# Optimization experiments

Hardware: AMD Instinct MI355X
Metric: run time of the kernel (lower is better)

Reference implementation:

```python
import jax, jax.numpy as jnp
import numpy as np

K = 5
TAU = 2.0
EPS = 1e-8
SLOPE = 0.2  # LeakyReLU negative slope
BASE = jnp.array([-2.0, -1.0, 0.0, 1.0, 2.0], dtype=jnp.float32)


def _leaky(x):
    return jnp.where(x >= 0, x, SLOPE * x)


def _bilinear1d(feat, x):
    """1D bilinear sample, equivalent to F.grid_sample on an [B,C,1,L] image
    with grid_y=0, padding_mode='border', align_corners=True.
    feat: [B,C,L], x: [B,M] normalized coords in [-1,1]. Returns [B,C,M]."""
    L = feat.shape[-1]
    ix = jnp.clip((x + 1.0) * 0.5 * (L - 1), 0.0, float(L - 1))  # border clamp
    x0 = jnp.floor(ix)
    w = (ix - x0)[:, None, :]  # [B,1,M]
    i0 = jnp.clip(x0.astype(jnp.int32), 0, L - 1)
    i1 = jnp.clip(i0 + 1, 0, L - 1)
    f0 = jnp.take_along_axis(feat, i0[:, None, :], axis=2)
    f1 = jnp.take_along_axis(feat, i1[:, None, :], axis=2)
    return f0 * (1.0 - w) + f1 * w


def setup_inputs() -> dict:
    key = jax.random.key(0)
    ks = jax.random.split(key, 10)
    B, C, Lin, N, H = 4, 256, 4096, 8192, 64
    out_dim = 1 + 1 + K + K  # 12
    feat_1d = jax.random.normal(ks[0], (B, C, Lin), dtype=jnp.float32)
    coords_1d = jax.random.uniform(ks[1], (B, N, 1), minval=-1.0, maxval=1.0, dtype=jnp.float32)
    cell_1d = jnp.full((B, N, 1), 2.0 / Lin, dtype=jnp.float32) * (1.0 + 0.1 * jax.random.uniform(ks[2], (B, N, 1)))
    in_dim = C + 2
    # NOTE: original zero-inits the last linear; we use small random weights to
    # exercise the full computation (non-degenerate offsets/gates).
    W1 = jax.random.normal(ks[3], (in_dim, H), dtype=jnp.float32) * (1.0 / np.sqrt(in_dim))
    b1 = jax.random.normal(ks[4], (H,), dtype=jnp.float32) * 0.01
    Wr = jax.random.normal(ks[5], (H, H), dtype=jnp.float32) * (1.0 / np.sqrt(H))
    br = jax.random.normal(ks[6], (H,), dtype=jnp.float32) * 0.01
    W3 = jax.random.normal(ks[7], (H, out_dim), dtype=jnp.float32) * 0.1
    b3 = jax.random.normal(ks[8], (out_dim,), dtype=jnp.float32) * 0.01
    return {"feat_1d": feat_1d, "coords_1d": coords_1d, "cell_1d": cell_1d,
            "W1": W1, "b1": b1, "Wr": Wr, "br": br, "W3": W3, "b3": b3}


def reference(feat_1d, coords_1d, cell_1d, W1, b1, Wr, br, W3, b3):
    B, C, Lin = feat_1d.shape
    N = coords_1d.shape[1]
    x = coords_1d[..., 0]  # [B,N]
    # anchor features at query coords
    f_anchor = _bilinear1d(feat_1d, x).transpose(0, 2, 1)  # [B,N,C]
    rin = jnp.concatenate([f_anchor, coords_1d, cell_1d], axis=-1)  # [B,N,C+2]
    # router MLP: Linear -> LeakyReLU -> ResidualBlock -> Linear
    h = _leaky(rin @ W1 + b1)
    h = _leaky(h + (h @ Wr + br))
    out = h @ W3 + b3  # [B,N,12]
    r_raw = out[..., 0:1]
    sigma_raw = out[..., 1:2]
    res_raw = out[..., 2:2 + K]
    gate_raw = out[..., 2 + K:2 + 2 * K]
    r = jnp.clip(jax.nn.softplus(r_raw) + 0.3, 0.3, 2.0)          # [B,N,1]
    sigma = jnp.clip(jax.nn.softplus(sigma_raw) + 0.5, 0.5, 3.0)  # [B,N,1]
    res = jnp.tanh(res_raw) * 0.5                                  # [B,N,K]
    off = r * BASE + res                                           # [B,N,K] pixel-unit offsets
    scale_x = 2.0 / max(Lin - 1, 1)
    deform_x = x[:, :, None] + off * scale_x                       # [B,N,K] normalized
    f = _bilinear1d(feat_1d, deform_x.reshape(B, N * K))           # [B,C,N*K]
    f = f.reshape(B, C, N, K).transpose(0, 2, 3, 1)                # [B,N,K,C]
    w_geo = jnp.exp(-0.5 * off ** 2 / ((sigma * TAU) ** 2 + EPS))  # [B,N,K]
    w = w_geo * jax.nn.sigmoid(gate_raw)
    w = w / (w.sum(axis=-1, keepdims=True) + EPS)
    out_feat = jnp.einsum('bnkc,bnk->bnc', f, w)                   # [B,N,C]
    return out_feat
```

## Files before the change

### kernel.cpp

```cpp
#include <hip/hip_runtime.h>
#include <math.h>

#define KK 5
#define C_DIM 256
#define LIN 4096
#define B_DIM 4
#define N_PTS 8192
#define PTS 32
#define NBUCK (B_DIM * LIN)
#define WROWS 32
#define SROWS 44

typedef short short8 __attribute__((ext_vector_type(8)));
typedef float f32x4  __attribute__((ext_vector_type(4)));

__device__ __forceinline__ float leaky(float v) { return v >= 0.0f ? v : 0.2f * v; }
__device__ __forceinline__ float softplus_f(float v) { return v > 20.0f ? v : log1pf(expf(v)); }
__device__ __forceinline__ float bflo(unsigned u) { return __uint_as_float(u << 16); }
__device__ __forceinline__ float bfhi(unsigned u) { return __uint_as_float(u & 0xFFFF0000u); }
__device__ __forceinline__ ushort f2bf(float f) {
    unsigned u = __float_as_uint(f);
    u += 0x7FFFu + ((u >> 16) & 1u);
    return (ushort)(u >> 16);
}
__device__ __forceinline__ float bf2f(ushort h) { return __uint_as_float((unsigned)h << 16); }
__device__ __forceinline__ int anchor_key(const float* coords, int pt) {
    float x = coords[pt];
    float ix = fminf(fmaxf((x + 1.0f) * 0.5f * (float)(LIN - 1), 0.0f), (float)(LIN - 1));
    return (pt >> 13) * LIN + (int)ix;
}

__global__ __launch_bounds__(256) void prep_weights(
    const float* __restrict__ W1, const float* __restrict__ Wr,
    ushort* __restrict__ W1t_hi, ushort* __restrict__ W1t_lo,
    ushort* __restrict__ Wrt_hi, ushort* __restrict__ Wrt_lo)
{
    int i = blockIdx.x * 256 + threadIdx.x;
    if (i < 64 * 264) {
        int j = i / 264, k = i % 264;
        float v = (k < 256) ? W1[(size_t)k * 64 + j] : 0.0f;
        ushort hi = f2bf(v);
        W1t_hi[i] = hi;
        W1t_lo[i] = f2bf(v - bf2f(hi));
    } else {
        int i2 = i - 64 * 264;
        if (i2 < 64 * 72) {
            int j = i2 / 72, k = i2 % 72;
            float v = (k < 64) ? Wr[(size_t)k * 64 + j] : 0.0f;
            ushort hi = f2bf(v);
            Wrt_hi[i2] = hi;
            Wrt_lo[i2] = f2bf(v - bf2f(hi));
        }
    }
}

__global__ __launch_bounds__(256) void sort_count(
    const float* __restrict__ coords, unsigned* __restrict__ hist)
{
    int pt = blockIdx.x * 256 + threadIdx.x;
    atomicAdd(&hist[anchor_key(coords, pt)], 1u);
}

__global__ __launch_bounds__(256) void sort_scan(
    const unsigned* __restrict__ hist, unsigned* __restrict__ offs,
    unsigned* __restrict__ pfx)
{
    __shared__ unsigned base[256];
    int t = threadIdx.x;
    unsigned s = 0;
    for (int i = 0; i < NBUCK / 256; i++) s += hist[t * (NBUCK / 256) + i];
    base[t] = s;
    __syncthreads();
    if (t == 0) {
        unsigned run = 0;
        for (int i = 0; i < 256; i++) { unsigned v = base[i]; base[i] = run; run += v; }
    }
    __syncthreads();
    unsigned run = base[t];
    for (int i = 0; i < NBUCK / 256; i++) {
        int idx = t * (NBUCK / 256) + i;
        offs[idx] = run;
        pfx[idx] = run;
        run += hist[idx];
    }
    if (t == 255) pfx[NBUCK] = run;
}

__global__ __launch_bounds__(256) void sort_scatter(
    const float* __restrict__ coords, unsigned* __restrict__ offs,
    int* __restrict__ perm)
{
    int pt = blockIdx.x * 256 + threadIdx.x;
    unsigned pos = atomicAdd(&offs[anchor_key(coords, pt)], 1u);
    perm[pos] = pt;
}

__global__ __launch_bounds__(256) void transpose_kernel(
    const float* __restrict__ feat, ushort* __restrict__ feat_t)
{
    __shared__ float tile[64][33];
    int b  = blockIdx.z;
    int l0 = blockIdx.x * 32;
    int c0 = blockIdx.y * 64;
    const float* src = feat + (size_t)b * C_DIM * LIN;
    unsigned* dst = (unsigned*)(feat_t + (size_t)b * LIN * C_DIM);
    int tx = threadIdx.x, ty = threadIdx.y;
#pragma unroll
    for (int i = 0; i < 8; i++)
        tile[ty + i * 8][tx] = src[(size_t)(c0 + ty + i * 8) * LIN + (l0 + tx)];
    __syncthreads();
#pragma unroll
    for (int i = 0; i < 4; i++) {
        int l = ty + i * 8;
        unsigned lo = f2bf(tile[2 * tx][l]);
        unsigned hi = f2bf(tile[2 * tx + 1][l]);
        dst[((size_t)(l0 + l) * C_DIM + c0) / 2 + tx] = lo | (hi << 16);
    }
}

__global__ __launch_bounds__(256) void mlp_kernel(
    const ushort* __restrict__ feat_t,
    const float* __restrict__ coords,
    const float* __restrict__ cell,
    const float* __restrict__ W1, const float* __restrict__ b1,
    const float* __restrict__ br,
    const float* __restrict__ W3, const float* __restrict__ b3,
    const ushort* __restrict__ W1t_hi, const ushort* __restrict__ W1t_lo,
    const ushort* __restrict__ Wrt_hi, const ushort* __restrict__ Wrt_lo,
    const int* __restrict__ perm,
    float* __restrict__ params)
{
    __shared__ ushort Ah[PTS][264], Al[PTS][264];
    __shared__ ushort H1h[PTS][72], H1l[PTS][72];
    __shared__ float  H2[PTS][68];
    __shared__ float  outs[PTS][12];
    __shared__ float  xs[PTS], cls[PTS];

    const int t = threadIdx.x;
    const int base = blockIdx.x * PTS;
    const int bb = base >> 13;
    const ushort* fb = feat_t + (size_t)bb * LIN * C_DIM;

    {
        int p = t >> 3, l8 = t & 7;
        int pt = perm[base + p];
        float x = coords[pt];
        float ix = fminf(fmaxf((x + 1.0f) * 0.5f * (float)(LIN - 1), 0.0f), (float)(LIN - 1));
        float x0 = floorf(ix);
        int i0 = min((int)x0, LIN - 1);
        int i1 = min(i0 + 1, LIN - 1);
        float fr = ix - x0, om = 1.0f - fr;
        if (l8 == 0) { xs[p] = x; cls[p] = cell[pt]; }
        const ushort* r0 = fb + (size_t)i0 * C_DIM;
        const ushort* r1 = fb + (size_t)i1 * C_DIM;
#pragma unroll
        for (int q = 0; q < 4; q++) {
            int c = l8 * 8 + q * 64;
            uint4 u0 = *(const uint4*)(r0 + c);
            uint4 u1 = *(const uint4*)(r1 + c);
            float v[8];
            v[0] = bflo(u0.x) * om + bflo(u1.x) * fr;
            v[1] = bfhi(u0.x) * om + bfhi(u1.x) * fr;
            v[2] = bflo(u0.y) * om + bflo(u1.y) * fr;
            v[3] = bfhi(u0.y) * om + bfhi(u1.y) * fr;
            v[4] = bflo(u0.z) * om + bflo(u1.z) * fr;
            v[5] = bfhi(u0.z) * om + bfhi(u1.z) * fr;
            v[6] = bflo(u0.w) * om + bflo(u1.w) * fr;
            v[7] = bfhi(u0.w) * om + bfhi(u1.w) * fr;
            ushort hv[8], lv[8];
#pragma unroll
            for (int e = 0; e < 8; e++) {
                hv[e] = f2bf(v[e]);
                lv[e] = f2bf(v[e] - bf2f(hv[e]));
            }
            *(uint4*)&Ah[p][c] = *(uint4*)hv;
            *(uint4*)&Al[p][c] = *(uint4*)lv;
        }
    }
    __syncthreads();

    const int wave = t >> 6, lane = t & 63;
    const int cr = lane & 15;
    const int kb = lane >> 4;
    const int jcol = wave * 16 + cr;

    f32x4 acc0 = {0.f, 0.f, 0.f, 0.f}, acc1 = acc0;
    {
        const ushort* B1h = W1t_hi + (size_t)jcol * 264;
        const ushort* B1l = W1t_lo + (size_t)jcol * 264;
#pragma unroll
        for (int k0 = 0; k0 < 256; k0 += 32) {
            int ko = k0 + kb * 8;
            short8 a0h = *(const short8*)&Ah[cr][ko];
            short8 a0l = *(const short8*)&Al[cr][ko];
            short8 a1h = *(const short8*)&Ah[16 + cr][ko];
            short8 a1l = *(const short8*)&Al[16 + cr][ko];
            short8 bh = *(const short8*)(B1h + ko);
            short8 bl = *(const short8*)(B1l + ko);
            acc0 = __builtin_amdgcn_mfma_f32_16x16x32_bf16(a0h, bh, acc0, 0, 0, 0);
            acc0 = __builtin_amdgcn_mfma_f32_16x16x32_bf16(a0h, bl, acc0, 0, 0, 0);
            acc0 = __builtin_amdgcn_mfma_f32_16x16x32_bf16(a0l, bh, acc0, 0, 0, 0);
            acc1 = __builtin_amdgcn_mfma_f32_16x16x32_bf16(a1h, bh, acc1, 0, 0, 0);
            acc1 = __builtin_amdgcn_mfma_f32_16x16x32_bf16(a1h, bl, acc1, 0, 0, 0);
            acc1 = __builtin_amdgcn_mfma_f32_16x16x32_bf16(a1l, bh, acc1, 0, 0, 0);
        }
    }
    float h1a[4], h1b[4];
    {
        float wx = W1[(size_t)256 * 64 + jcol];
        float wc = W1[(size_t)257 * 64 + jcol];
        float bb1 = b1[jcol];
#pragma unroll
        for (int r = 0; r < 4; r++) {
            int p0 = kb * 4 + r;
            float v0 = leaky(acc0[r] + xs[p0] * wx + cls[p0] * wc + bb1);
            h1a[r] = v0;
            ushort hi0 = f2bf(v0);
            H1h[p0][jcol] = hi0;
            H1l[p0][jcol] = f2bf(v0 - bf2f(hi0));
            int p1 = 16 + p0;
            float v1 = leaky(acc1[r] + xs[p1] * wx + cls[p1] * wc + bb1);
            h1b[r] = v1;
            ushort hi1 = f2bf(v1);
            H1h[p1][jcol] = hi1;
            H1l[p1][jcol] = f2bf(v1 - bf2f(hi1));
        }
    }
    __syncthreads();

    f32x4 r0 = {0.f, 0.f, 0.f, 0.f}, r1 = r0;
    {
        const ushort* B2h = Wrt_hi + (size_t)jcol * 72;
        const ushort* B2l = Wrt_lo + (size_t)jcol * 72;
#pragma unroll
        for (int k0 = 0; k0 < 64; k0 += 32) {
            int ko = k0 + kb * 8;
            short8 a0h = *(const short8*)&H1h[cr][ko];
            short8 a0l = *(const short8*)&H1l[cr][ko];
            short8 a1h = *(const short8*)&H1h[16 + cr][ko];
            short8 a1l = *(const short8*)&H1l[16 + cr][ko];
            short8 bh = *(const short8*)(B2h + ko);
            short8 bl = *(const short8*)(B2l + ko);
            r0 = __builtin_amdgcn_mfma_f32_16x16x32_bf16(a0h, bh, r0, 0, 0, 0);
            r0 = __builtin_amdgcn_mfma_f32_16x16x32_bf16(a0h, bl, r0, 0, 0, 0);
            r0 = __builtin_amdgcn_mfma_f32_16x16x32_bf16(a0l, bh, r0, 0, 0, 0);
            r1 = __builtin_amdgcn_mfma_f32_16x16x32_bf16(a1h, bh, r1, 0, 0, 0);
            r1 = __builtin_amdgcn_mfma_f32_16x16x32_bf16(a1h, bl, r1, 0, 0, 0);
            r1 = __builtin_amdgcn_mfma_f32_16x16x32_bf16(a1l, bh, r1, 0, 0, 0);
        }
        float brv = br[jcol];
#pragma unroll
        for (int r = 0; r < 4; r++) {
            int p0 = kb * 4 + r;
            H2[p0][jcol]      = leaky(h1a[r] + r0[r] + brv);
            H2[16 + p0][jcol] = leaky(h1b[r] + r1[r] + brv);
        }
    }
    __syncthreads();

    {
        int p = t & 31;
        int o = t >> 5;
        for (int oo = o; oo < 12; oo += 8) {
            float acc = b3[oo];
#pragma unroll 4
            for (int l = 0; l < 64; l++)
                acc = fmaf(H2[p][l], W3[(size_t)l * 12 + oo], acc);
            outs[p][oo] = acc;
        }
    }
    __syncthreads();

    if (t < PTS) {
        int pt = perm[base + t];
        float x = xs[t];
        float r = softplus_f(outs[t][0]) + 0.3f;
        r = fminf(fmaxf(r, 0.3f), 2.0f);
        float sg = softplus_f(outs[t][1]) + 0.5f;
        sg = fminf(fmaxf(sg, 0.5f), 3.0f);
        float denom = (sg * 2.0f) * (sg * 2.0f) + 1e-8f;
        const float BASEv[KK] = {-2.0f, -1.0f, 0.0f, 1.0f, 2.0f};
        float ixk[KK], wk[KK];
        float wsum = 0.0f;
#pragma unroll
        for (int k = 0; k < KK; k++) {
            float res = tanhf(outs[t][2 + k]) * 0.5f;
            float off = r * BASEv[k] + res;
            float dx = x + off * (2.0f / (float)(LIN - 1));
            float ix = (dx + 1.0f) * 0.5f * (float)(LIN - 1);
            ix = fminf(fmaxf(ix, 0.0f), (float)(LIN - 1));
            float gate = outs[t][2 + KK + k];
            float wgeo = expf(-0.5f * off * off / denom);
            float sig = 1.0f / (1.0f + expf(-gate));
            float w = wgeo * sig;
            ixk[k] = ix; wk[k] = w; wsum += w;
        }
        float inv = 1.0f / (wsum + 1e-8f);
        float* pp = params + (size_t)pt * 10;
#pragma unroll
        for (int k = 0; k < KK; k++) {
            pp[k]     = ixk[k];
            pp[5 + k] = wk[k] * inv;
        }
    }
}

__global__ __launch_bounds__(256) void gather_kernel(
    const ushort* __restrict__ feat_t, const float* __restrict__ params,
    const int* __restrict__ perm, const unsigned* __restrict__ pfx,
    float* __restrict__ out)
{
    __shared__ uint4 sm[SROWS * 32];
    const int t = threadIdx.x;
    const int wpb = LIN / WROWS;
    const int b  = blockIdx.x / wpb;
    const int w0 = (blockIdx.x % wpb) * WROWS;
    const int rowLo = max(0, w0 - 5);
    const int rowHi = min(LIN, w0 + WROWS + 6);
    const int nrows = rowHi - rowLo;

    const uint4* src = (const uint4*)(feat_t + ((size_t)b * LIN + rowLo) * C_DIM);
    for (int i = t; i < nrows * 32; i += 256) sm[i] = src[i];
    __syncthreads();

    const unsigned ptStart = pfx[b * LIN + w0];
    const unsigned ptEnd   = pfx[b * LIN + w0 + WROWS];
    const int lane = t & 31;

    for (unsigned ip = ptStart + (t >> 5); ip < ptEnd; ip += 8) {
        int pt = perm[ip];
        const float* pp = params + (size_t)pt * 10;
        float a0 = 0, a1 = 0, a2 = 0, a3 = 0, a4 = 0, a5 = 0, a6 = 0, a7 = 0;
#pragma unroll
        for (int k = 0; k < KK; k++) {
            float ix = pp[k];
            float w  = pp[5 + k];
            float x0 = floorf(ix);
            int i0 = (int)x0;
            int i1 = min(i0 + 1, LIN - 1);
            float fr = ix - x0;
            uint4 u0 = sm[(i0 - rowLo) * 32 + lane];
            uint4 u1 = sm[(i1 - rowLo) * 32 + lane];
            float w0f = w * (1.0f - fr), w1f = w * fr;
            a0 = fmaf(w0f, bflo(u0.x), fmaf(w1f, bflo(u1.x), a0));
            a1 = fmaf(w0f, bfhi(u0.x), fmaf(w1f, bfhi(u1.x), a1));
            a2 = fmaf(w0f, bflo(u0.y), fmaf(w1f, bflo(u1.y), a2));
            a3 = fmaf(w0f, bfhi(u0.y), fmaf(w1f, bfhi(u1.y), a3));
            a4 = fmaf(w0f, bflo(u0.z), fmaf(w1f, bflo(u1.z), a4));
            a5 = fmaf(w0f, bfhi(u0.z), fmaf(w1f, bfhi(u1.z), a5));
            a6 = fmaf(w0f, bflo(u0.w), fmaf(w1f, bflo(u1.w), a6));
            a7 = fmaf(w0f, bfhi(u0.w), fmaf(w1f, bfhi(u1.w), a7));
        }
        float* op = out + (size_t)pt * C_DIM + lane * 8;
        *(float4*)op       = make_float4(a0, a1, a2, a3);
        *(float4*)(op + 4) = make_float4(a4, a5, a6, a7);
    }
}

extern "C" void kernel_launch(void* const* d_in, const int* in_sizes, int n_in,
                              void* d_out, int out_size, void* d_ws, size_t ws_size,
                              hipStream_t stream) {
    const float* feat   = (const float*)d_in[0];
    const float* coords = (const float*)d_in[1];
    const float* cell   = (const float*)d_in[2];
    const float* W1 = (const float*)d_in[3];
    const float* b1 = (const float*)d_in[4];
    const float* Wr = (const float*)d_in[5];
    const float* br = (const float*)d_in[6];
    const float* W3 = (const float*)d_in[7];
    const float* b3 = (const float*)d_in[8];
    float* out = (float*)d_out;

    char* ws = (char*)d_ws;
    ushort* feat_t = (ushort*)ws;
    ws += (size_t)B_DIM * LIN * C_DIM * 2;
    float* params = (float*)ws;
    ws += (size_t)B_DIM * N_PTS * 10 * 4;
    ushort* W1t_hi = (ushort*)ws; ws += 64 * 264 * 2;
    ushort* W1t_lo = (ushort*)ws; ws += 64 * 264 * 2;
    ushort* Wrt_hi = (ushort*)ws; ws += 64 * 72 * 2;
    ushort* Wrt_lo = (ushort*)ws; ws += 64 * 72 * 2;
    ws = (char*)(((uintptr_t)ws + 255) & ~(uintptr_t)255);
    unsigned* hist = (unsigned*)ws; ws += NBUCK * 4;
    unsigned* offs = (unsigned*)ws; ws += NBUCK * 4;
    unsigned* pfx  = (unsigned*)ws; ws += (NBUCK + 1) * 4;
    ws = (char*)(((uintptr_t)ws + 255) & ~(uintptr_t)255);
    int* perm      = (int*)ws;      ws += (size_t)B_DIM * N_PTS * 4;

    int nPts = B_DIM * N_PTS;

    hipMemsetAsync(hist, 0, NBUCK * 4, stream);
    sort_count<<<nPts / 256, 256, 0, stream>>>(coords, hist);
    sort_scan<<<1, 256, 0, stream>>>(hist, offs, pfx);
    sort_scatter<<<nPts / 256, 256, 0, stream>>>(coords, offs, perm);

    prep_weights<<<(64 * 264 + 64 * 72 + 255) / 256, 256, 0, stream>>>(
        W1, Wr, W1t_hi, W1t_lo, Wrt_hi, Wrt_lo);

    dim3 tb(32, 8);
    dim3 tg(LIN / 32, C_DIM / 64, B_DIM);
    transpose_kernel<<<tg, tb, 0, stream>>>(feat, feat_t);

    mlp_kernel<<<nPts / PTS, 256, 0, stream>>>(feat_t, coords, cell,
                                               W1, b1, br, W3, b3,
                                               W1t_hi, W1t_lo, Wrt_hi, Wrt_lo,
                                               perm, params);

    gather_kernel<<<B_DIM * (LIN / WROWS), 256, 0, stream>>>(
        feat_t, params, perm, pfx, out);
}
```

Before: 149.8 us.

## Fuse transpose, MLP router and gather into one window-tiled kernel

Replaces the separate transpose, MLP and gather kernels with one kernel per 32-row window. Each block loads a halo of the feature rows straight from the original fp32 layout into shared memory as bf16. It then runs the router MLP in 32-point chunks and does the deformable gather from that shared tile. This removes the global bf16 transposed feature buffer, the params round trip and two launches. The costs are strided per-channel global reads when filling the tile, extra barriers per chunk, and uneven work per block depending on how many points fall into each window.

```diff
diff --git a/kernel.cpp b/kernel.cpp
--- a/kernel.cpp
+++ b/kernel.cpp
@@ -10,6 +10,7 @@
 #define NBUCK (B_DIM * LIN)
 #define WROWS 32
 #define SROWS 44
+#define WPB (LIN / WROWS)
 
 typedef short short8 __attribute__((ext_vector_type(8)));
 typedef float f32x4  __attribute__((ext_vector_type(4)));
@@ -95,31 +96,8 @@
     perm[pos] = pt;
 }
 
-__global__ __launch_bounds__(256) void transpose_kernel(
-    const float* __restrict__ feat, ushort* __restrict__ feat_t)
-{
-    __shared__ float tile[64][33];
-    int b  = blockIdx.z;
-    int l0 = blockIdx.x * 32;
-    int c0 = blockIdx.y * 64;
-    const float* src = feat + (size_t)b * C_DIM * LIN;
-    unsigned* dst = (unsigned*)(feat_t + (size_t)b * LIN * C_DIM);
-    int tx = threadIdx.x, ty = threadIdx.y;
-#pragma unroll
-    for (int i = 0; i < 8; i++)
-        tile[ty + i * 8][tx] = src[(size_t)(c0 + ty + i * 8) * LIN + (l0 + tx)];
-    __syncthreads();
-#pragma unroll
-    for (int i = 0; i < 4; i++) {
-        int l = ty + i * 8;
-        unsigned lo = f2bf(tile[2 * tx][l]);
-        unsigned hi = f2bf(tile[2 * tx + 1][l]);
-        dst[((size_t)(l0 + l) * C_DIM + c0) / 2 + tx] = lo | (hi << 16);
-    }
-}
-
-__global__ __launch_bounds__(256) void mlp_kernel(
-    const ushort* __restrict__ feat_t,
+__global__ __launch_bounds__(256) void fused_kernel(
+    const float* __restrict__ feat,
     const float* __restrict__ coords,
     const float* __restrict__ cell,
     const float* __restrict__ W1, const float* __restrict__ b1,
@@ -127,89 +105,108 @@
     const float* __restrict__ W3, const float* __restrict__ b3,
     const ushort* __restrict__ W1t_hi, const ushort* __restrict__ W1t_lo,
     const ushort* __restrict__ Wrt_hi, const ushort* __restrict__ Wrt_lo,
-    const int* __restrict__ perm,
-    float* __restrict__ params)
-{
+    const int* __restrict__ perm, const unsigned* __restrict__ pfx,
+    float* __restrict__ out)
+{
+    __shared__ ushort fs[SROWS][264];
     __shared__ ushort Ah[PTS][264], Al[PTS][264];
     __shared__ ushort H1h[PTS][72], H1l[PTS][72];
     __shared__ float  H2[PTS][68];
     __shared__ float  outs[PTS][12];
+    __shared__ float  sxw[PTS][10];
     __shared__ float  xs[PTS], cls[PTS];
+    __shared__ int    pts[PTS];
 
     const int t = threadIdx.x;
-    const int base = blockIdx.x * PTS;
-    const int bb = base >> 13;
-    const ushort* fb = feat_t + (size_t)bb * LIN * C_DIM;
+    const int b  = blockIdx.x / WPB;
+    const int w0 = (blockIdx.x % WPB) * WROWS;
+    const int rowLo = max(0, w0 - 5);
+    const int rowHi = min(LIN, w0 + WROWS + 6);
+    const int nrows = rowHi - rowLo;
 
     {
-        int p = t >> 3, l8 = t & 7;
-        int pt = perm[base + p];
-        float x = coords[pt];
-        float ix = fminf(fmaxf((x + 1.0f) * 0.5f * (float)(LIN - 1), 0.0f), (float)(LIN - 1));
-        float x0 = floorf(ix);
-        int i0 = min((int)x0, LIN - 1);
-        int i1 = min(i0 + 1, LIN - 1);
-        float fr = ix - x0, om = 1.0f - fr;
-        if (l8 == 0) { xs[p] = x; cls[p] = cell[pt]; }
-        const ushort* r0 = fb + (size_t)i0 * C_DIM;
-        const ushort* r1 = fb + (size_t)i1 * C_DIM;
-#pragma unroll
-        for (int q = 0; q < 4; q++) {
-            int c = l8 * 8 + q * 64;
-            uint4 u0 = *(const uint4*)(r0 + c);
-            uint4 u1 = *(const uint4*)(r1 + c);
-            float v[8];
-            v[0] = bflo(u0.x) * om + bflo(u1.x) * fr;
-            v[1] = bfhi(u0.x) * om + bfhi(u1.x) * fr;
-            v[2] = bflo(u0.y) * om + bflo(u1.y) * fr;
-            v[3] = bfhi(u0.y) * om + bfhi(u1.y) * fr;
-            v[4] = bflo(u0.z) * om + bflo(u1.z) * fr;
-            v[5] = bfhi(u0.z) * om + bfhi(u1.z) * fr;
-            v[6] = bflo(u0.w) * om + bflo(u1.w) * fr;
-            v[7] = bfhi(u0.w) * om + bfhi(u1.w) * fr;
-            ushort hv[8], lv[8];
-#pragma unroll
-            for (int e = 0; e < 8; e++) {
-                hv[e] = f2bf(v[e]);
-                lv[e] = f2bf(v[e] - bf2f(hv[e]));
-            }
-            *(uint4*)&Ah[p][c] = *(uint4*)hv;
-            *(uint4*)&Al[p][c] = *(uint4*)lv;
-        }
-    }
-    __syncthreads();
+        const float* fsrc = feat + ((size_t)b * C_DIM + t) * LIN + rowLo;
+        for (int l = 0; l < nrows; l++)
+            fs[l][t] = f2bf(fsrc[l]);
+    }
+
+    const unsigned ptStart = pfx[b * LIN + w0];
+    const unsigned ptEnd   = pfx[b * LIN + w0 + WROWS];
 
     const int wave = t >> 6, lane = t & 63;
     const int cr = lane & 15;
     const int kb = lane >> 4;
     const int jcol = wave * 16 + cr;
-
-    f32x4 acc0 = {0.f, 0.f, 0.f, 0.f}, acc1 = acc0;
-    {
-        const ushort* B1h = W1t_hi + (size_t)jcol * 264;
-        const ushort* B1l = W1t_lo + (size_t)jcol * 264;
-#pragma unroll
-        for (int k0 = 0; k0 < 256; k0 += 32) {
-            int ko = k0 + kb * 8;
-            short8 a0h = *(const short8*)&Ah[cr][ko];
-            short8 a0l = *(const short8*)&Al[cr][ko];
-            short8 a1h = *(const short8*)&Ah[16 + cr][ko];
-            short8 a1l = *(const short8*)&Al[16 + cr][ko];
-            short8 bh = *(const short8*)(B1h + ko);
-            short8 bl = *(const short8*)(B1l + ko);
-            acc0 = __builtin_amdgcn_mfma_f32_16x16x32_bf16(a0h, bh, acc0, 0, 0, 0);
-            acc0 = __builtin_amdgcn_mfma_f32_16x16x32_bf16(a0h, bl, acc0, 0, 0, 0);
-            acc0 = __builtin_amdgcn_mfma_f32_16x16x32_bf16(a0l, bh, acc0, 0, 0, 0);
-            acc1 = __builtin_amdgcn_mfma_f32_16x16x32_bf16(a1h, bh, acc1, 0, 0, 0);
-            acc1 = __builtin_amdgcn_mfma_f32_16x16x32_bf16(a1h, bl, acc1, 0, 0, 0);
-            acc1 = __builtin_amdgcn_mfma_f32_16x16x32_bf16(a1l, bh, acc1, 0, 0, 0);
-        }
-    }
-    float h1a[4], h1b[4];
-    {
-        float wx = W1[(size_t)256 * 64 + jcol];
-        float wc = W1[(size_t)257 * 64 + jcol];
-        float bb1 = b1[jcol];
+    const float wx  = W1[(size_t)256 * 64 + jcol];
+    const float wc  = W1[(size_t)257 * 64 + jcol];
+    const float bb1 = b1[jcol];
+    const float brv = br[jcol];
+
+    for (unsigned chunkBase = ptStart; chunkBase < ptEnd; chunkBase += PTS) {
+        const int npts = (int)min((unsigned)PTS, ptEnd - chunkBase);
+        __syncthreads();
+        if (t < PTS) pts[t] = perm[chunkBase + min(t, npts - 1)];
+        __syncthreads();
+
+        {
+            int p = t >> 3, l8 = t & 7;
+            int pt = pts[p];
+            float x = coords[pt];
+            float ix = fminf(fmaxf((x + 1.0f) * 0.5f * (float)(LIN - 1), 0.0f), (float)(LIN - 1));
+            float x0 = floorf(ix);
+            int i0 = min((int)x0, LIN - 1);
+            int i1 = min(i0 + 1, LIN - 1);
+            float fr = ix - x0, om = 1.0f - fr;
+            int r0 = i0 - rowLo, r1 = i1 - rowLo;
+            if (l8 == 0) { xs[p] = x; cls[p] = cell[pt]; }
+#pragma unroll
+            for (int q = 0; q < 4; q++) {
+                int c = l8 * 8 + q * 64;
+                uint4 u0 = *(const uint4*)&fs[r0][c];
+                uint4 u1 = *(const uint4*)&fs[r1][c];
+                float v[8];
+                v[0] = bflo(u0.x) * om + bflo(u1.x) * fr;
+                v[1] = bfhi(u0.x) * om + bfhi(u1.x) * fr;
+                v[2] = bflo(u0.y) * om + bflo(u1.y) * fr;
+                v[3] = bfhi(u0.y) * om + bfhi(u1.y) * fr;
+                v[4] = bflo(u0.z) * om + bflo(u1.z) * fr;
+                v[5] = bfhi(u0.z) * om + bfhi(u1.z) * fr;
+                v[6] = bflo(u0.w) * om + bflo(u1.w) * fr;
+                v[7] = bfhi(u0.w) * om + bfhi(u1.w) * fr;
+                ushort hv[8], lv[8];
+#pragma unroll
+                for (int e = 0; e < 8; e++) {
+                    hv[e] = f2bf(v[e]);
+                    lv[e] = f2bf(v[e] - bf2f(hv[e]));
+                }
+                *(uint4*)&Ah[p][c] = *(uint4*)hv;
+                *(uint4*)&Al[p][c] = *(uint4*)lv;
+            }
+        }
+        __syncthreads();
+
+        f32x4 acc0 = {0.f, 0.f, 0.f, 0.f}, acc1 = acc0;
+        {
+            const ushort* B1h = W1t_hi + (size_t)jcol * 264;
+            const ushort* B1l = W1t_lo + (size_t)jcol * 264;
+#pragma unroll
+            for (int k0 = 0; k0 < 256; k0 += 32) {
+                int ko = k0 + kb * 8;
+                short8 a0h = *(const short8*)&Ah[cr][ko];
+                short8 a0l = *(const short8*)&Al[cr][ko];
+                short8 a1h = *(const short8*)&Ah[16 + cr][ko];
+                short8 a1l = *(const short8*)&Al[16 + cr][ko];
+                short8 bh = *(const short8*)(B1h + ko);
+                short8 bl = *(const short8*)(B1l + ko);
+                acc0 = __builtin_amdgcn_mfma_f32_16x16x32_bf16(a0h, bh, acc0, 0, 0, 0);
+                acc0 = __builtin_amdgcn_mfma_f32_16x16x32_bf16(a0h, bl, acc0, 0, 0, 0);
+                acc0 = __builtin_amdgcn_mfma_f32_16x16x32_bf16(a0l, bh, acc0, 0, 0, 0);
+                acc1 = __builtin_amdgcn_mfma_f32_16x16x32_bf16(a1h, bh, acc1, 0, 0, 0);
+                acc1 = __builtin_amdgcn_mfma_f32_16x16x32_bf16(a1h, bl, acc1, 0, 0, 0);
+                acc1 = __builtin_amdgcn_mfma_f32_16x16x32_bf16(a1l, bh, acc1, 0, 0, 0);
+            }
+        }
+        float h1a[4], h1b[4];
 #pragma unroll
         for (int r = 0; r < 4; r++) {
             int p0 = kb * 4 + r;
@@ -225,135 +222,111 @@
             H1h[p1][jcol] = hi1;
             H1l[p1][jcol] = f2bf(v1 - bf2f(hi1));
         }
-    }
-    __syncthreads();
-
-    f32x4 r0 = {0.f, 0.f, 0.f, 0.f}, r1 = r0;
-    {
-        const ushort* B2h = Wrt_hi + (size_t)jcol * 72;
-        const ushort* B2l = Wrt_lo + (size_t)jcol * 72;
-#pragma unroll
-        for (int k0 = 0; k0 < 64; k0 += 32) {
-            int ko = k0 + kb * 8;
-            short8 a0h = *(const short8*)&H1h[cr][ko];
-            short8 a0l = *(const short8*)&H1l[cr][ko];
-            short8 a1h = *(const short8*)&H1h[16 + cr][ko];
-            short8 a1l = *(const short8*)&H1l[16 + cr][ko];
-            short8 bh = *(const short8*)(B2h + ko);
-            short8 bl = *(const short8*)(B2l + ko);
-            r0 = __builtin_amdgcn_mfma_f32_16x16x32_bf16(a0h, bh, r0, 0, 0, 0);
-            r0 = __builtin_amdgcn_mfma_f32_16x16x32_bf16(a0h, bl, r0, 0, 0, 0);
-            r0 = __builtin_amdgcn_mfma_f32_16x16x32_bf16(a0l, bh, r0, 0, 0, 0);
-            r1 = __builtin_amdgcn_mfma_f32_16x16x32_bf16(a1h, bh, r1, 0, 0, 0);
-            r1 = __builtin_amdgcn_mfma_f32_16x16x32_bf16(a1h, bl, r1, 0, 0, 0);
-            r1 = __builtin_amdgcn_mfma_f32_16x16x32_bf16(a1l, bh, r1, 0, 0, 0);
-        }
-        float brv = br[jcol];
-#pragma unroll
-        for (int r = 0; r < 4; r++) {
-            int p0 = kb * 4 + r;
-            H2[p0][jcol]      = leaky(h1a[r] + r0[r] + brv);
-            H2[16 + p0][jcol] = leaky(h1b[r] + r1[r] + brv);
-        }
-    }
-    __syncthreads();
-
-    {
-        int p = t & 31;
-        int o = t >> 5;
-        for (int oo = o; oo < 12; oo += 8) {
-            float acc = b3[oo];
+        __syncthreads();
+
+        {
+            f32x4 r0 = {0.f, 0.f, 0.f, 0.f}, r1 = r0;
+            const ushort* B2h = Wrt_hi + (size_t)jcol * 72;
+            const ushort* B2l = Wrt_lo + (size_t)jcol * 72;
+#pragma unroll
+            for (int k0 = 0; k0 < 64; k0 += 32) {
+                int ko = k0 + kb * 8;
+                short8 a0h = *(const short8*)&H1h[cr][ko];
+                short8 a0l = *(const short8*)&H1l[cr][ko];
+                short8 a1h = *(const short8*)&H1h[16 + cr][ko];
+                short8 a1l = *(const short8*)&H1l[16 + cr][ko];
+                short8 bh = *(const short8*)(B2h + ko);
+                short8 bl = *(const short8*)(B2l + ko);
+                r0 = __builtin_amdgcn_mfma_f32_16x16x32_bf16(a0h, bh, r0, 0, 0, 0);
+                r0 = __builtin_amdgcn_mfma_f32_16x16x32_bf16(a0h, bl, r0, 0, 0, 0);
+                r0 = __builtin_amdgcn_mfma_f32_16x16x32_bf16(a0l, bh, r0, 0, 0, 0);
+                r1 = __builtin_amdgcn_mfma_f32_16x16x32_bf16(a1h, bh, r1, 0, 0, 0);
+                r1 = __builtin_amdgcn_mfma_f32_16x16x32_bf16(a1h, bl, r1, 0, 0, 0);
+                r1 = __builtin_amdgcn_mfma_f32_16x16x32_bf16(a1l, bh, r1, 0, 0, 0);
+            }
+#pragma unroll
+            for (int r = 0; r < 4; r++) {
+                int p0 = kb * 4 + r;
+                H2[p0][jcol]      = leaky(h1a[r] + r0[r] + brv);
+                H2[16 + p0][jcol] = leaky(h1b[r] + r1[r] + brv);
+            }
+        }
+        __syncthreads();
+
+        {
+            int p = t & 31;
+            int o = t >> 5;
+            for (int oo = o; oo < 12; oo += 8) {
+                float acc = b3[oo];
 #pragma unroll 4
-            for (int l = 0; l < 64; l++)
-                acc = fmaf(H2[p][l], W3[(size_t)l * 12 + oo], acc);
-            outs[p][oo] = acc;
-        }
-    }
-    __syncthreads();
-
-    if (t < PTS) {
-        int pt = perm[base + t];
-        float x = xs[t];
-        float r = softplus_f(outs[t][0]) + 0.3f;
-        r = fminf(fmaxf(r, 0.3f), 2.0f);
-        float sg = softplus_f(outs[t][1]) + 0.5f;
-        sg = fminf(fmaxf(sg, 0.5f), 3.0f);
-        float denom = (sg * 2.0f) * (sg * 2.0f) + 1e-8f;
-        const float BASEv[KK] = {-2.0f, -1.0f, 0.0f, 1.0f, 2.0f};
-        float ixk[KK], wk[KK];
-        float wsum = 0.0f;
-#pragma unroll
-        for (int k = 0; k < KK; k++) {
-            float res = tanhf(outs[t][2 + k]) * 0.5f;
-            float off = r * BASEv[k] + res;
-            float dx = x + off * (2.0f / (float)(LIN - 1));
-            float ix = (dx + 1.0f) * 0.5f * (float)(LIN - 1);
-            ix = fminf(fmaxf(ix, 0.0f), (float)(LIN - 1));
-            float gate = outs[t][2 + KK + k];
-            float wgeo = expf(-0.5f * off * off / denom);
-            float sig = 1.0f / (1.0f + expf(-gate));
-            float w = wgeo * sig;
-            ixk[k] = ix; wk[k] = w; wsum += w;
-        }
-        float inv = 1.0f / (wsum + 1e-8f);
-        float* pp = params + (size_t)pt * 10;
-#pragma unroll
-        for (int k = 0; k < KK; k++) {
-            pp[k]     = ixk[k];
-            pp[5 + k] = wk[k] * inv;
-        }
-    }
-}
-
-__global__ __launch_bounds__(256) void gather_kernel(
-    const ushort* __restrict__ feat_t, const float* __restrict__ params,
-    const int* __restrict__ perm, const unsigned* __restrict__ pfx,
-    float* __restrict__ out)
-{
-    __shared__ uint4 sm[SROWS * 32];
-    const int t = threadIdx.x;
-    const int wpb = LIN / WROWS;
-    const int b  = blockIdx.x / wpb;
-    const int w0 = (blockIdx.x % wpb) * WROWS;
-    const int rowLo = max(0, w0 - 5);
-    const int rowHi = min(LIN, w0 + WROWS + 6);
-    const int nrows = rowHi - rowLo;
-
-    const uint4* src = (const uint4*)(feat_t + ((size_t)b * LIN + rowLo) * C_DIM);
-    for (int i = t; i < nrows * 32; i += 256) sm[i] = src[i];
-    __syncthreads();
-
-    const unsigned ptStart = pfx[b * LIN + w0];
-    const unsigned ptEnd   = pfx[b * LIN + w0 + WROWS];
-    const int lane = t & 31;
-
-    for (unsigned ip = ptStart + (t >> 5); ip < ptEnd; ip += 8) {
-        int pt = perm[ip];
-        const float* pp = params + (size_t)pt * 10;
-        float a0 = 0, a1 = 0, a2 = 0, a3 = 0, a4 = 0, a5 = 0, a6 = 0, a7 = 0;
-#pragma unroll
-        for (int k = 0; k < KK; k++) {
-            float ix = pp[k];
-            float w  = pp[5 + k];
-            float x0 = floorf(ix);
-            int i0 = (int)x0;
-            int i1 = min(i0 + 1, LIN - 1);
-            float fr = ix - x0;
-            uint4 u0 = sm[(i0 - rowLo) * 32 + lane];
-            uint4 u1 = sm[(i1 - rowLo) * 32 + lane];
-            float w0f = w * (1.0f - fr), w1f = w * fr;
-            a0 = fmaf(w0f, bflo(u0.x), fmaf(w1f, bflo(u1.x), a0));
-            a1 = fmaf(w0f, bfhi(u0.x), fmaf(w1f, bfhi(u1.x), a1));
-            a2 = fmaf(w0f, bflo(u0.y), fmaf(w1f, bflo(u1.y), a2));
-            a3 = fmaf(w0f, bfhi(u0.y), fmaf(w1f, bfhi(u1.y), a3));
-            a4 = fmaf(w0f, bflo(u0.z), fmaf(w1f, bflo(u1.z), a4));
-            a5 = fmaf(w0f, bfhi(u0.z), fmaf(w1f, bfhi(u1.z), a5));
-            a6 = fmaf(w0f, bflo(u0.w), fmaf(w1f, bflo(u1.w), a6));
-            a7 = fmaf(w0f, bfhi(u0.w), fmaf(w1f, bfhi(u1.w), a7));
-        }
-        float* op = out + (size_t)pt * C_DIM + lane * 8;
-        *(float4*)op       = make_float4(a0, a1, a2, a3);
-        *(float4*)(op + 4) = make_float4(a4, a5, a6, a7);
+                for (int l = 0; l < 64; l++)
+                    acc = fmaf(H2[p][l], W3[(size_t)l * 12 + oo], acc);
+                outs[p][oo] = acc;
+            }
+        }
+        __syncthreads();
+
+        if (t < PTS) {
+            float x = xs[t];
+            float r = softplus_f(outs[t][0]) + 0.3f;
+            r = fminf(fmaxf(r, 0.3f), 2.0f);
+            float sg = softplus_f(outs[t][1]) + 0.5f;
+            sg = fminf(fmaxf(sg, 0.5f), 3.0f);
+            float denom = (sg * 2.0f) * (sg * 2.0f) + 1e-8f;
+            const float BASEv[KK] = {-2.0f, -1.0f, 0.0f, 1.0f, 2.0f};
+            float wk[KK];
+            float wsum = 0.0f;
+#pragma unroll
+            for (int k = 0; k < KK; k++) {
+                float res = tanhf(outs[t][2 + k]) * 0.5f;
+                float off = r * BASEv[k] + res;
+                float dx = x + off * (2.0f / (float)(LIN - 1));
+                float ix = (dx + 1.0f) * 0.5f * (float)(LIN - 1);
+                ix = fminf(fmaxf(ix, 0.0f), (float)(LIN - 1));
+                float gate = outs[t][2 + KK + k];
+                float wgeo = expf(-0.5f * off * off / denom);
+                float sig = 1.0f / (1.0f + expf(-gate));
+                float w = wgeo * sig;
+                sxw[t][k] = ix;
+                wk[k] = w; wsum += w;
+            }
+            float inv = 1.0f / (wsum + 1e-8f);
+#pragma unroll
+            for (int k = 0; k < KK; k++) sxw[t][5 + k] = wk[k] * inv;
+        }
+        __syncthreads();
+
+        {
+            int worker = t >> 5, gl = t & 31;
+            int c = gl * 8;
+            for (int p = worker; p < npts; p += 8) {
+                int pt = pts[p];
+                float a0 = 0, a1 = 0, a2 = 0, a3 = 0, a4 = 0, a5 = 0, a6 = 0, a7 = 0;
+#pragma unroll
+                for (int k = 0; k < KK; k++) {
+                    float ix = sxw[p][k];
+                    float w  = sxw[p][5 + k];
+                    float x0 = floorf(ix);
+                    int i0 = (int)x0;
+                    int i1 = min(i0 + 1, LIN - 1);
+                    float fr = ix - x0;
+                    uint4 u0 = *(const uint4*)&fs[i0 - rowLo][c];
+                    uint4 u1 = *(const uint4*)&fs[i1 - rowLo][c];
+                    float w0f = w * (1.0f - fr), w1f = w * fr;
+                    a0 = fmaf(w0f, bflo(u0.x), fmaf(w1f, bflo(u1.x), a0));
+                    a1 = fmaf(w0f, bfhi(u0.x), fmaf(w1f, bfhi(u1.x), a1));
+                    a2 = fmaf(w0f, bflo(u0.y), fmaf(w1f, bflo(u1.y), a2));
+                    a3 = fmaf(w0f, bfhi(u0.y), fmaf(w1f, bfhi(u1.y), a3));
+                    a4 = fmaf(w0f, bflo(u0.z), fmaf(w1f, bflo(u1.z), a4));
+                    a5 = fmaf(w0f, bfhi(u0.z), fmaf(w1f, bfhi(u1.z), a5));
+                    a6 = fmaf(w0f, bflo(u0.w), fmaf(w1f, bflo(u1.w), a6));
+                    a7 = fmaf(w0f, bfhi(u0.w), fmaf(w1f, bfhi(u1.w), a7));
+                }
+                float* op = out + (size_t)pt * C_DIM + c;
+                *(float4*)op       = make_float4(a0, a1, a2, a3);
+                *(float4*)(op + 4) = make_float4(a4, a5, a6, a7);
+            }
+        }
     }
 }
 
@@ -372,10 +345,6 @@
     float* out = (float*)d_out;
 
     char* ws = (char*)d_ws;
-    ushort* feat_t = (ushort*)ws;
-    ws += (size_t)B_DIM * LIN * C_DIM * 2;
-    float* params = (float*)ws;
-    ws += (size_t)B_DIM * N_PTS * 10 * 4;
     ushort* W1t_hi = (ushort*)ws; ws += 64 * 264 * 2;
     ushort* W1t_lo = (ushort*)ws; ws += 64 * 264 * 2;
     ushort* Wrt_hi = (ushort*)ws; ws += 64 * 72 * 2;
@@ -397,15 +366,7 @@
     prep_weights<<<(64 * 264 + 64 * 72 + 255) / 256, 256, 0, stream>>>(
         W1, Wr, W1t_hi, W1t_lo, Wrt_hi, Wrt_lo);
 
-    dim3 tb(32, 8);
-    dim3 tg(LIN / 32, C_DIM / 64, B_DIM);
-    transpose_kernel<<<tg, tb, 0, stream>>>(feat, feat_t);
-
-    mlp_kernel<<<nPts / PTS, 256, 0, stream>>>(feat_t, coords, cell,
-                                               W1, b1, br, W3, b3,
-                                               W1t_hi, W1t_lo, Wrt_hi, Wrt_lo,
-                                               perm, params);
-
-    gather_kernel<<<B_DIM * (LIN / WROWS), 256, 0, stream>>>(
-        feat_t, params, perm, pfx, out);
-}
+    fused_kernel<<<B_DIM * WPB, 256, 0, stream>>>(
+        feat, coords, cell, W1, b1, br, W3, b3,
+        W1t_hi, W1t_lo, Wrt_hi, Wrt_lo, perm, pfx, out);
+}
```

New measurement: 148.4 us. About the same (-0.9%).
